# Kernel tuning notes

Measured on AMD Instinct MI355X. Metric: run time of the kernel, lower is better.

The kernel has to match this reference:

```python
import jax, jax.numpy as jnp
import numpy as np

N_NODES = 50000
N_EDGES = 800000
IN_DIM = 128
HID = 128
OUT_DIM = 64
NUM_GRAPHS = 512
GM_P = 2.0
EPS = 1e-6


def setup_inputs() -> dict:
    key = jax.random.key(0)
    ks = jax.random.split(key, 12)
    x = jax.random.normal(ks[0], (N_NODES, IN_DIM), dtype=jnp.float32)
    edge_index = jax.random.randint(ks[1], (2, N_EDGES), 0, N_NODES, dtype=jnp.int64)
    batch = jnp.sort(jax.random.randint(ks[2], (N_NODES,), 0, NUM_GRAPHS, dtype=jnp.int64))
    def lin(k, fan_in, fan_out):
        w = jax.random.normal(k, (fan_in, fan_out), dtype=jnp.float32) / np.sqrt(fan_in)
        return w
    return {
        "x": x,
        "edge_index": edge_index,
        "batch": batch,
        # 3 GCN conv layers (weight + bias each)
        "W0": lin(ks[3], IN_DIM, HID), "b0": jnp.zeros((HID,), jnp.float32),
        "W1": lin(ks[4], HID, HID),    "b1": jnp.zeros((HID,), jnp.float32),
        "W2": lin(ks[5], HID, HID),    "b2": jnp.zeros((HID,), jnp.float32),
        # 2 FF layers: [HID->HID], [HID->OUT_DIM]
        "Wf0": lin(ks[6], HID, HID),   "bf0": jnp.zeros((HID,), jnp.float32),
        "Wf1": lin(ks[7], HID, OUT_DIM), "bf1": jnp.zeros((OUT_DIM,), jnp.float32),
    }


def _gcn_layer(h, src, dst, deg_inv_sqrt, W, b):
    # PyG GCNConv: h' = D^-1/2 (A + I) D^-1/2 (h W) + b, deg includes self-loop
    h = h @ W                                           # [N, F]
    norm = deg_inv_sqrt[src] * deg_inv_sqrt[dst]        # [E]
    msg = h[src] * norm[:, None]                        # gather + scale, [E, F]
    agg = jax.ops.segment_sum(msg, dst, num_segments=N_NODES)
    agg = agg + h * (deg_inv_sqrt * deg_inv_sqrt)[:, None]   # self-loop term (norm = 1/deg)
    return agg + b


def _gm_pool(x, batch, p):
    # sign-preserving generalized mean pool via scatter_mean
    xt = jnp.sign(x) * (jnp.abs(x) + EPS) ** p
    sums = jax.ops.segment_sum(xt, batch, num_segments=NUM_GRAPHS)
    cnt = jax.ops.segment_sum(jnp.ones((x.shape[0],), x.dtype), batch, num_segments=NUM_GRAPHS)
    pooled = sums / jnp.maximum(cnt, 1.0)[:, None]
    return jnp.sign(pooled) * (jnp.abs(pooled) + EPS) ** (1.0 / p)


def reference(x, edge_index, batch, W0, b0, W1, b1, W2, b2, Wf0, bf0, Wf1, bf1):
    src, dst = edge_index[0], edge_index[1]
    # degree of aggregation targets, with +1 for self-loops (computed once; graph is static)
    deg = jax.ops.segment_sum(jnp.ones((N_EDGES,), x.dtype), dst, num_segments=N_NODES) + 1.0
    deg_inv_sqrt = jax.lax.rsqrt(deg)

    h = _gcn_layer(x, src, dst, deg_inv_sqrt, W0, b0)
    h = jax.nn.relu(h)
    h = _gcn_layer(h, src, dst, deg_inv_sqrt, W1, b1)
    h = jax.nn.relu(h)
    h = _gcn_layer(h, src, dst, deg_inv_sqrt, W2, b2)  # no relu after last conv

    graph_repr = _gm_pool(h, batch, GM_P)              # [G, HID]
    graph_repr = jax.nn.relu(graph_repr)

    z = jax.nn.relu(graph_repr @ Wf0 + bf0)
    logits = z @ Wf1 + bf1                             # [G, OUT_DIM]
    return logits
```

## Files before the change

### kernel.cpp

```cpp
#include <hip/hip_runtime.h>

#define N_NODES   50000
#define M_PAD     50048
#define N_TILES   1564
#define GEMM_GRID 391
#define N_EDGES   800000
#define HID       128
#define OUT_DIM   64
#define NUM_GRAPHS 512
#define EPS       1e-6f
#define NBUCK     196
#define BUCKCAP   6144
#define ABLOCKS   98

typedef __attribute__((ext_vector_type(8))) short short8;
typedef __attribute__((ext_vector_type(4))) float f32x4;
typedef __attribute__((ext_vector_type(16))) float f32x16;

static __device__ __forceinline__ unsigned short f2bf(float f) {
    unsigned u = __builtin_bit_cast(unsigned, f);
    u += 0x7FFFu + ((u >> 16) & 1u);
    return (unsigned short)(u >> 16);
}
static __device__ __forceinline__ float bf2f(unsigned short h) {
    unsigned u = ((unsigned)h) << 16;
    return __builtin_bit_cast(float, u);
}

static __device__ __forceinline__ float signpow(float x, bool sqrt_mode) {
    if (x == 0.0f) return 0.0f;
    float a = fabsf(x) + EPS;
    float v = sqrt_mode ? sqrtf(a) : a * a;
    return x > 0.0f ? v : -v;
}

__global__ __launch_bounds__(256) void k_bucketize(const int* __restrict__ ei,
                                                   int* __restrict__ gcnt,
                                                   unsigned* __restrict__ ebuf) {
    __shared__ int lcnt[NBUCK];
    __shared__ int lbase[NBUCK];
    int tid = threadIdx.x;
    for (int i = tid; i < NBUCK; i += 256) lcnt[i] = 0;
    __syncthreads();

    const uint4* src4 = (const uint4*)ei;
    const uint4* dst4 = (const uint4*)(ei + N_EDGES);
    int base4 = blockIdx.x * 2048;

    #pragma unroll 1
    for (int it = 0; it < 8; it++) {
        int i4 = base4 + it * 256 + tid;
        if (i4 < N_EDGES / 4) {
            uint4 d = dst4[i4];
            atomicAdd(&lcnt[d.x >> 8], 1);
            atomicAdd(&lcnt[d.y >> 8], 1);
            atomicAdd(&lcnt[d.z >> 8], 1);
            atomicAdd(&lcnt[d.w >> 8], 1);
        }
    }
    __syncthreads();
    for (int i = tid; i < NBUCK; i += 256) {
        lbase[i] = atomicAdd(&gcnt[i], lcnt[i]);
        lcnt[i] = 0;
    }
    __syncthreads();

    #pragma unroll 1
    for (int it = 0; it < 8; it++) {
        int i4 = base4 + it * 256 + tid;
        if (i4 < N_EDGES / 4) {
            uint4 d = dst4[i4];
            uint4 s = src4[i4];
            unsigned dd[4] = {d.x, d.y, d.z, d.w};
            unsigned ss[4] = {s.x, s.y, s.z, s.w};
            #pragma unroll
            for (int k = 0; k < 4; k++) {
                int b = dd[k] >> 8;
                int p = atomicAdd(&lcnt[b], 1);
                ebuf[(size_t)b * BUCKCAP + lbase[b] + p] = ss[k] | (dd[k] << 16);
            }
        }
    }
}

__global__ __launch_bounds__(256) void k_bscan(const int* __restrict__ gcnt,
                                               int* __restrict__ bbase,
                                               int* __restrict__ offs) {
    __shared__ int sm[256];
    int t = threadIdx.x;
    int v = (t < NBUCK) ? gcnt[t] : 0;
    sm[t] = v;
    __syncthreads();
    for (int off = 1; off < 256; off <<= 1) {
        int u = (t >= off) ? sm[t - off] : 0;
        __syncthreads();
        sm[t] += u;
        __syncthreads();
    }
    if (t < NBUCK) bbase[t] = sm[t] - v;
    if (t == 0) { bbase[NBUCK] = N_EDGES; offs[N_NODES] = N_EDGES; }
}

__global__ __launch_bounds__(256) void k_csr(const unsigned* __restrict__ ebuf,
                                             const int* __restrict__ gcnt,
                                             const int* __restrict__ bbase,
                                             int* __restrict__ offs,
                                             float* __restrict__ dis,
                                             int* __restrict__ csr) {
    __shared__ int cntA[256];
    __shared__ int scanA[256];
    int b = blockIdx.x;
    int t = threadIdx.x;
    int n0 = b * 256;
    int count = gcnt[b];
    int base  = bbase[b];
    const unsigned* eb = ebuf + (size_t)b * BUCKCAP;

    cntA[t] = 0;
    __syncthreads();
    for (int i = t; i < count; i += 256)
        atomicAdd(&cntA[eb[i] >> 16 & 0xFF], 1);
    __syncthreads();
    int c = cntA[t];
    scanA[t] = c;
    __syncthreads();
    for (int off = 1; off < 256; off <<= 1) {
        int u = (t >= off) ? scanA[t - off] : 0;
        __syncthreads();
        scanA[t] += u;
        __syncthreads();
    }
    int excl = scanA[t] - c;
    int n = n0 + t;
    if (n < N_NODES) {
        offs[n] = base + excl;
        dis[n]  = rsqrtf((float)c + 1.0f);
    }
    scanA[t] = excl;
    cntA[t] = 0;
    __syncthreads();
    for (int i = t; i < count; i += 256) {
        unsigned v = eb[i];
        int ln = (v >> 16) & 0xFF;
        int p = atomicAdd(&cntA[ln], 1);
        csr[base + scanA[ln] + p] = (int)(v & 0xFFFFu);
    }
}

__global__ void k_split(const float* __restrict__ in, short* __restrict__ hi,
                        short* __restrict__ lo, int n4) {
    int i = blockIdx.x * blockDim.x + threadIdx.x;
    if (i >= n4) return;
    float4 v = ((const float4*)in)[i];
    unsigned short h0 = f2bf(v.x), h1 = f2bf(v.y), h2 = f2bf(v.z), h3 = f2bf(v.w);
    unsigned short l0 = f2bf(v.x - bf2f(h0)), l1 = f2bf(v.y - bf2f(h1));
    unsigned short l2 = f2bf(v.z - bf2f(h2)), l3 = f2bf(v.w - bf2f(h3));
    ushort4 vh; vh.x = h0; vh.y = h1; vh.z = h2; vh.w = h3;
    ushort4 vl; vl.x = l0; vl.y = l1; vl.z = l2; vl.w = l3;
    ((ushort4*)hi)[i] = vh;
    ((ushort4*)lo)[i] = vl;
}

__global__ void k_wsplit3(const float* __restrict__ W0, const float* __restrict__ W1,
                          const float* __restrict__ W2, short* __restrict__ Wth,
                          short* __restrict__ Wtl) {
    int which = blockIdx.y;
    const float* W = which == 0 ? W0 : (which == 1 ? W1 : W2);
    int tid = blockIdx.x * blockDim.x + threadIdx.x;
    int k = tid & 127, n = tid >> 7;
    float w = W[k * HID + n];
    unsigned short h = f2bf(w);
    Wth[which * HID * HID + n * HID + k] = (short)h;
    Wtl[which * HID * HID + n * HID + k] = (short)f2bf(w - bf2f(h));
}

__global__ __launch_bounds__(256) void k_gemm_mfma(const short* __restrict__ Ah,
                                                   const short* __restrict__ Al,
                                                   const short* __restrict__ Wh,
                                                   const short* __restrict__ Wl,
                                                   unsigned short* __restrict__ th,
                                                   unsigned short* __restrict__ tl,
                                                   const float* __restrict__ scale) {
    __shared__ short As_h[32 * 128];
    __shared__ short As_l[32 * 128];
    int tid  = threadIdx.x;
    int lane = tid & 63;
    int col  = (tid >> 6) * 32 + (lane & 31);
    int kh   = lane >> 5;
    int r    = lane & 31;

    short8 bh[8], bl[8];
    #pragma unroll
    for (int ks = 0; ks < 8; ks++) {
        bh[ks] = *(const short8*)(Wh + (size_t)col * HID + ks * 16 + kh * 8);
        bl[ks] = *(const short8*)(Wl + (size_t)col * HID + ks * 16 + kh * 8);
    }

    int su0 = tid, su1 = tid + 256;
    int sr0 = su0 >> 4, sc0 = su0 & 15;
    int sr1 = su1 >> 4, sc1 = su1 & 15;
    int sw0 = sr0 * 128 + ((sc0 ^ (sr0 & 7)) * 8);
    int sw1 = sr1 * 128 + ((sc1 ^ (sr1 & 7)) * 8);

    for (int tile = blockIdx.x; tile < N_TILES; tile += GEMM_GRID) {
        int row0 = tile * 32;
        __syncthreads();
        {
            const short* gh = Ah + (size_t)row0 * HID;
            const short* gl = Al + (size_t)row0 * HID;
            *(short8*)&As_h[sw0] = *(const short8*)(gh + sr0 * HID + sc0 * 8);
            *(short8*)&As_h[sw1] = *(const short8*)(gh + sr1 * HID + sc1 * 8);
            *(short8*)&As_l[sw0] = *(const short8*)(gl + sr0 * HID + sc0 * 8);
            *(short8*)&As_l[sw1] = *(const short8*)(gl + sr1 * HID + sc1 * 8);
        }
        __syncthreads();

        short8 ah[8], al[8];
        #pragma unroll
        for (int ks = 0; ks < 8; ks++) {
            int cg = ks * 2 + kh;
            int off = r * 128 + ((cg ^ (r & 7)) * 8);
            ah[ks] = *(const short8*)&As_h[off];
            al[ks] = *(const short8*)&As_l[off];
        }

        f32x16 acc = {0.f};
        #pragma unroll
        for (int ks = 0; ks < 8; ks++) {
            acc = __builtin_amdgcn_mfma_f32_32x32x16_bf16(ah[ks], bh[ks], acc, 0, 0, 0);
            acc = __builtin_amdgcn_mfma_f32_32x32x16_bf16(al[ks], bh[ks], acc, 0, 0, 0);
            acc = __builtin_amdgcn_mfma_f32_32x32x16_bf16(ah[ks], bl[ks], acc, 0, 0, 0);
        }

        #pragma unroll
        for (int reg = 0; reg < 16; reg++) {
            int row = row0 + (reg & 3) + 8 * (reg >> 2) + 4 * kh;
            float v = acc[reg] * scale[row];
            unsigned short hi = f2bf(v);
            th[(size_t)row * HID + col] = hi;
            tl[(size_t)row * HID + col] = f2bf(v - bf2f(hi));
        }
    }
}

__global__ __launch_bounds__(256) void k_agg(const unsigned short* __restrict__ th,
                                             const unsigned short* __restrict__ tl,
                                             const int* __restrict__ offs,
                                             const int* __restrict__ csr_src,
                                             const float* __restrict__ dis,
                                             const float* __restrict__ bias,
                                             float* __restrict__ hout,
                                             short* __restrict__ hh,
                                             short* __restrict__ hl,
                                             int mode) {
    int node = blockIdx.x * 4 + (threadIdx.x >> 6);
    if (node >= N_NODES) return;
    int lane = threadIdx.x & 63;
    int c  = lane & 31;
    int e  = lane >> 5;
    int beg = offs[node], end = offs[node + 1];
    float dn = dis[node];

    float ax[4] = {}, ay[4] = {}, az[4] = {}, aw[4] = {};
    for (int j = beg; j < end; j += 8) {
        #pragma unroll
        for (int k = 0; k < 4; k++) {
            int jj = j + k * 2 + e;
            int jc = jj < end ? jj : end - 1;
            int s = csr_src[jc];
            float m = (jj < end) ? 1.0f : 0.0f;
            uint2 v = *(const uint2*)&th[(size_t)s * HID + c * 4];
            float v0 = __builtin_bit_cast(float, v.x << 16);
            float v1 = __builtin_bit_cast(float, v.x & 0xFFFF0000u);
            float v2 = __builtin_bit_cast(float, v.y << 16);
            float v3 = __builtin_bit_cast(float, v.y & 0xFFFF0000u);
            ax[k] = fmaf(v0, m, ax[k]);
            ay[k] = fmaf(v1, m, ay[k]);
            az[k] = fmaf(v2, m, az[k]);
            aw[k] = fmaf(v3, m, aw[k]);
        }
    }
    float tx = (ax[0] + ax[1]) + (ax[2] + ax[3]);
    float ty = (ay[0] + ay[1]) + (ay[2] + ay[3]);
    float tz = (az[0] + az[1]) + (az[2] + az[3]);
    float tw = (aw[0] + aw[1]) + (aw[2] + aw[3]);
    tx += __shfl_xor(tx, 32);
    ty += __shfl_xor(ty, 32);
    tz += __shfl_xor(tz, 32);
    tw += __shfl_xor(tw, 32);

    if (e == 0) {
        ushort4 sh = *(const ushort4*)&th[(size_t)node * HID + c * 4];
        ushort4 sl = *(const ushort4*)&tl[(size_t)node * HID + c * 4];
        float4 b4  = *(const float4*)&bias[c * 4];
        float ox = (tx + bf2f(sh.x) + bf2f(sl.x)) * dn + b4.x;
        float oy = (ty + bf2f(sh.y) + bf2f(sl.y)) * dn + b4.y;
        float oz = (tz + bf2f(sh.z) + bf2f(sl.z)) * dn + b4.z;
        float ow = (tw + bf2f(sh.w) + bf2f(sl.w)) * dn + b4.w;
        if (mode == 1) {
            ox = fmaxf(ox, 0.f); oy = fmaxf(oy, 0.f);
            oz = fmaxf(oz, 0.f); ow = fmaxf(ow, 0.f);
            unsigned short hx = f2bf(ox), hy = f2bf(oy), hz = f2bf(oz), hw = f2bf(ow);
            ushort4 vh; vh.x = hx; vh.y = hy; vh.z = hz; vh.w = hw;
            ushort4 vl;
            vl.x = f2bf(ox - bf2f(hx)); vl.y = f2bf(oy - bf2f(hy));
            vl.z = f2bf(oz - bf2f(hz)); vl.w = f2bf(ow - bf2f(hw));
            *(ushort4*)&hh[(size_t)node * HID + c * 4] = vh;
            *(ushort4*)&hl[(size_t)node * HID + c * 4] = vl;
        } else {
            float4 o = make_float4(ox, oy, oz, ow);
            *(float4*)&hout[(size_t)node * HID + c * 4] = o;
        }
    }
}

__global__ void k_bounds(const int* __restrict__ batch, int* __restrict__ gstart) {
    int n = blockIdx.x * blockDim.x + threadIdx.x;
    if (n >= N_NODES) return;
    int b  = batch[n];
    int bp = (n == 0) ? -1 : batch[n - 1];
    for (int g = bp + 1; g <= b; g++) gstart[g] = n;
    if (n == N_NODES - 1)
        for (int g = b + 1; g <= NUM_GRAPHS; g++) gstart[g] = N_NODES;
}

__global__ __launch_bounds__(256) void k_pool(const float* __restrict__ h,
                                              const int* __restrict__ gstart,
                                              float* __restrict__ pooled) {
    __shared__ float smx[4][64], smy[4][64];
    int g = blockIdx.x;
    int t = threadIdx.x;
    int c = t & 63;
    int slot = t >> 6;
    int beg = gstart[g], end = gstart[g + 1];

    float sx = 0.f, sy = 0.f;
    for (int n = beg + slot; n < end; n += 4) {
        float2 v = *(const float2*)&h[(size_t)n * HID + c * 2];
        sx += signpow(v.x, false);
        sy += signpow(v.y, false);
    }
    smx[slot][c] = sx; smy[slot][c] = sy;
    __syncthreads();
    if (slot == 0) {
        sx = (smx[0][c] + smx[1][c]) + (smx[2][c] + smx[3][c]);
        sy = (smy[0][c] + smy[1][c]) + (smy[2][c] + smy[3][c]);
        float cnt = fmaxf((float)(end - beg), 1.0f);
        float px = sx / cnt, py = sy / cnt;
        pooled[g * HID + c * 2]     = fmaxf(signpow(px, true), 0.f);
        pooled[g * HID + c * 2 + 1] = fmaxf(signpow(py, true), 0.f);
    }
}

__global__ __launch_bounds__(128) void k_ff(const float* __restrict__ pooled,
                                            const float* __restrict__ Wf0,
                                            const float* __restrict__ bf0,
                                            const float* __restrict__ Wf1,
                                            const float* __restrict__ bf1,
                                            float* __restrict__ out) {
    __shared__ float row[128];
    __shared__ float zrow[128];
    int g = blockIdx.x, t = threadIdx.x;
    row[t] = pooled[g * HID + t];
    __syncthreads();
    float acc = bf0[t];
    #pragma unroll 8
    for (int k = 0; k < 128; k++) acc = fmaf(row[k], Wf0[k * 128 + t], acc);
    zrow[t] = fmaxf(acc, 0.f);
    __syncthreads();
    if (t < OUT_DIM) {
        float a2 = bf1[t];
        #pragma unroll 8
        for (int k = 0; k < 128; k++) a2 = fmaf(zrow[k], Wf1[k * OUT_DIM + t], a2);
        out[g * OUT_DIM + t] = a2;
    }
}

static inline size_t align256(size_t x) { return (x + 255) & ~(size_t)255; }

extern "C" void kernel_launch(void* const* d_in, const int* in_sizes, int n_in,
                              void* d_out, int out_size, void* d_ws, size_t ws_size,
                              hipStream_t stream) {
    const float* x     = (const float*)d_in[0];
    const int*   ei    = (const int*)d_in[1];
    const int*   batch = (const int*)d_in[2];
    const float* W0  = (const float*)d_in[3];  const float* b0  = (const float*)d_in[4];
    const float* W1  = (const float*)d_in[5];  const float* b1  = (const float*)d_in[6];
    const float* W2  = (const float*)d_in[7];  const float* b2  = (const float*)d_in[8];
    const float* Wf0 = (const float*)d_in[9];  const float* bf0 = (const float*)d_in[10];
    const float* Wf1 = (const float*)d_in[11]; const float* bf1 = (const float*)d_in[12];
    float* out = (float*)d_out;

    char* p = (char*)d_ws;
    unsigned short* th = (unsigned short*)p; p += align256((size_t)M_PAD * HID * 2);
    unsigned short* tl = (unsigned short*)p; p += align256((size_t)M_PAD * HID * 2);
    short* bufAh = (short*)p; p += align256((size_t)M_PAD * HID * 2);
    short* bufAl = (short*)p; p += align256((size_t)M_PAD * HID * 2);
    short* bufBh = (short*)p; p += align256((size_t)M_PAD * HID * 2);
    short* bufBl = (short*)p; p += align256((size_t)M_PAD * HID * 2);
    float* h     = (float*)bufBh;
    unsigned* ebuf = (unsigned*)p; p += align256((size_t)NBUCK * BUCKCAP * 4);
    int*   gcnt    = (int*)p;   p += align256((size_t)NBUCK * 4);
    int*   bbase   = (int*)p;   p += align256((size_t)(NBUCK + 1) * 4);
    int*   offs    = (int*)p;   p += align256((size_t)(N_NODES + 1) * 4);
    int*   csr     = (int*)p;   p += align256((size_t)N_EDGES * 4);
    float* dis     = (float*)p; p += align256((size_t)N_NODES * 4);
    int*   gstart  = (int*)p;   p += align256((size_t)(NUM_GRAPHS + 1) * 4);
    float* pooled  = (float*)p; p += align256((size_t)NUM_GRAPHS * HID * 4);
    short* Wth     = (short*)p; p += align256((size_t)3 * HID * HID * 2);
    short* Wtl     = (short*)p; p += align256((size_t)3 * HID * HID * 2);

    hipMemsetAsync(gcnt, 0, (size_t)NBUCK * 4, stream);

    const int TB = 256;
    k_bucketize<<<ABLOCKS, 256, 0, stream>>>(ei, gcnt, ebuf);
    k_bscan    <<<1, 256, 0, stream>>>(gcnt, bbase, offs);
    k_csr      <<<NBUCK, 256, 0, stream>>>(ebuf, gcnt, bbase, offs, dis, csr);

    int n4 = N_NODES * HID / 4;
    k_split<<<(n4 + TB - 1) / TB, TB, 0, stream>>>(x, bufAh, bufAl, n4);
    dim3 wg(64, 3);
    k_wsplit3<<<wg, 256, 0, stream>>>(W0, W1, W2, Wth, Wtl);

    int agg_blocks = (N_NODES + 3) / 4;

    k_gemm_mfma<<<GEMM_GRID, 256, 0, stream>>>(bufAh, bufAl, Wth, Wtl, th, tl, dis);
    k_agg<<<agg_blocks, 256, 0, stream>>>(th, tl, offs, csr, dis, b0,
                                          nullptr, bufBh, bufBl, 1);
    k_gemm_mfma<<<GEMM_GRID, 256, 0, stream>>>(bufBh, bufBl, Wth + HID * HID, Wtl + HID * HID,
                                               th, tl, dis);
    k_agg<<<agg_blocks, 256, 0, stream>>>(th, tl, offs, csr, dis, b1,
                                          nullptr, bufAh, bufAl, 1);
    k_gemm_mfma<<<GEMM_GRID, 256, 0, stream>>>(bufAh, bufAl, Wth + 2 * HID * HID, Wtl + 2 * HID * HID,
                                               th, tl, dis);
    k_agg<<<agg_blocks, 256, 0, stream>>>(th, tl, offs, csr, dis, b2,
                                          h, nullptr, nullptr, 0);

    k_bounds<<<(N_NODES + TB - 1) / TB, TB, 0, stream>>>(batch, gstart);
    k_pool<<<NUM_GRAPHS, 256, 0, stream>>>(h, gstart, pooled);
    k_ff<<<NUM_GRAPHS, 128, 0, stream>>>(pooled, Wf0, bf0, Wf1, bf1, out);
}
```

Baseline: 227.6 us.

## Fuse preprocessing kernels, drop low-bf16 GEMM output, fuse pool and FF

```diff
diff --git a/kernel.cpp b/kernel.cpp
--- a/kernel.cpp
+++ b/kernel.cpp
@@ -3,7 +3,7 @@
 #define N_NODES   50000
 #define M_PAD     50048
 #define N_TILES   1564
-#define GEMM_GRID 391
+#define GEMM_GRID 782
 #define N_EDGES   800000
 #define HID       128
 #define OUT_DIM   64
@@ -14,7 +14,6 @@
 #define ABLOCKS   98
 
 typedef __attribute__((ext_vector_type(8))) short short8;
-typedef __attribute__((ext_vector_type(4))) float f32x4;
 typedef __attribute__((ext_vector_type(16))) float f32x16;
 
 static __device__ __forceinline__ unsigned short f2bf(float f) {
@@ -83,37 +82,31 @@
     }
 }
 
-__global__ __launch_bounds__(256) void k_bscan(const int* __restrict__ gcnt,
-                                               int* __restrict__ bbase,
-                                               int* __restrict__ offs) {
-    __shared__ int sm[256];
-    int t = threadIdx.x;
-    int v = (t < NBUCK) ? gcnt[t] : 0;
-    sm[t] = v;
-    __syncthreads();
-    for (int off = 1; off < 256; off <<= 1) {
-        int u = (t >= off) ? sm[t - off] : 0;
-        __syncthreads();
-        sm[t] += u;
-        __syncthreads();
-    }
-    if (t < NBUCK) bbase[t] = sm[t] - v;
-    if (t == 0) { bbase[NBUCK] = N_EDGES; offs[N_NODES] = N_EDGES; }
-}
-
 __global__ __launch_bounds__(256) void k_csr(const unsigned* __restrict__ ebuf,
                                              const int* __restrict__ gcnt,
-                                             const int* __restrict__ bbase,
                                              int* __restrict__ offs,
                                              float* __restrict__ dis,
                                              int* __restrict__ csr) {
     __shared__ int cntA[256];
     __shared__ int scanA[256];
+    __shared__ int sbase;
     int b = blockIdx.x;
     int t = threadIdx.x;
     int n0 = b * 256;
+
+    int v = (t < NBUCK) ? gcnt[t] : 0;
+    scanA[t] = v;
+    __syncthreads();
+    for (int off = 1; off < 256; off <<= 1) {
+        int u = (t >= off) ? scanA[t - off] : 0;
+        __syncthreads();
+        scanA[t] += u;
+        __syncthreads();
+    }
+    if (t == 0) sbase = (b == 0) ? 0 : scanA[b - 1];
+    __syncthreads();
+    int base  = sbase;
     int count = gcnt[b];
-    int base  = bbase[b];
     const unsigned* eb = ebuf + (size_t)b * BUCKCAP;
 
     cntA[t] = 0;
@@ -136,29 +129,16 @@
         offs[n] = base + excl;
         dis[n]  = rsqrtf((float)c + 1.0f);
     }
+    if (b == 0 && t == 0) offs[N_NODES] = N_EDGES;
     scanA[t] = excl;
     cntA[t] = 0;
     __syncthreads();
     for (int i = t; i < count; i += 256) {
-        unsigned v = eb[i];
-        int ln = (v >> 16) & 0xFF;
+        unsigned vv = eb[i];
+        int ln = (vv >> 16) & 0xFF;
         int p = atomicAdd(&cntA[ln], 1);
-        csr[base + scanA[ln] + p] = (int)(v & 0xFFFFu);
-    }
-}
-
-__global__ void k_split(const float* __restrict__ in, short* __restrict__ hi,
-                        short* __restrict__ lo, int n4) {
-    int i = blockIdx.x * blockDim.x + threadIdx.x;
-    if (i >= n4) return;
-    float4 v = ((const float4*)in)[i];
-    unsigned short h0 = f2bf(v.x), h1 = f2bf(v.y), h2 = f2bf(v.z), h3 = f2bf(v.w);
-    unsigned short l0 = f2bf(v.x - bf2f(h0)), l1 = f2bf(v.y - bf2f(h1));
-    unsigned short l2 = f2bf(v.z - bf2f(h2)), l3 = f2bf(v.w - bf2f(h3));
-    ushort4 vh; vh.x = h0; vh.y = h1; vh.z = h2; vh.w = h3;
-    ushort4 vl; vl.x = l0; vl.y = l1; vl.z = l2; vl.w = l3;
-    ((ushort4*)hi)[i] = vh;
-    ((ushort4*)lo)[i] = vl;
+        csr[base + scanA[ln] + p] = (int)(vv & 0xFFFFu);
+    }
 }
 
 __global__ void k_wsplit3(const float* __restrict__ W0, const float* __restrict__ W1,
@@ -174,12 +154,12 @@
     Wtl[which * HID * HID + n * HID + k] = (short)f2bf(w - bf2f(h));
 }
 
-__global__ __launch_bounds__(256) void k_gemm_mfma(const short* __restrict__ Ah,
-                                                   const short* __restrict__ Al,
+template<int FP32SRC>
+__global__ __launch_bounds__(256) void k_gemm_mfma(const void* __restrict__ Asrc_h,
+                                                   const void* __restrict__ Asrc_l,
                                                    const short* __restrict__ Wh,
                                                    const short* __restrict__ Wl,
                                                    unsigned short* __restrict__ th,
-                                                   unsigned short* __restrict__ tl,
                                                    const float* __restrict__ scale) {
     __shared__ short As_h[32 * 128];
     __shared__ short As_l[32 * 128];
@@ -205,9 +185,29 @@
     for (int tile = blockIdx.x; tile < N_TILES; tile += GEMM_GRID) {
         int row0 = tile * 32;
         __syncthreads();
-        {
-            const short* gh = Ah + (size_t)row0 * HID;
-            const short* gl = Al + (size_t)row0 * HID;
+        if (FP32SRC) {
+            const float* gx = (const float*)Asrc_h;
+            #pragma unroll
+            for (int u = 0; u < 2; u++) {
+                int sr = u ? sr1 : sr0, sc = u ? sc1 : sc0, sw = u ? sw1 : sw0;
+                int gr = row0 + sr; if (gr >= N_NODES) gr = N_NODES - 1;
+                const float* src = gx + (size_t)gr * HID + sc * 8;
+                float4 a = ((const float4*)src)[0];
+                float4 b = ((const float4*)src)[1];
+                float vals[8] = {a.x, a.y, a.z, a.w, b.x, b.y, b.z, b.w};
+                short8 hi, lo;
+                #pragma unroll
+                for (int j = 0; j < 8; j++) {
+                    unsigned short hh = f2bf(vals[j]);
+                    hi[j] = (short)hh;
+                    lo[j] = (short)f2bf(vals[j] - bf2f(hh));
+                }
+                *(short8*)&As_h[sw] = hi;
+                *(short8*)&As_l[sw] = lo;
+            }
+        } else {
+            const short* gh = (const short*)Asrc_h + (size_t)row0 * HID;
+            const short* gl = (const short*)Asrc_l + (size_t)row0 * HID;
             *(short8*)&As_h[sw0] = *(const short8*)(gh + sr0 * HID + sc0 * 8);
             *(short8*)&As_h[sw1] = *(const short8*)(gh + sr1 * HID + sc1 * 8);
             *(short8*)&As_l[sw0] = *(const short8*)(gl + sr0 * HID + sc0 * 8);
@@ -236,15 +236,12 @@
         for (int reg = 0; reg < 16; reg++) {
             int row = row0 + (reg & 3) + 8 * (reg >> 2) + 4 * kh;
             float v = acc[reg] * scale[row];
-            unsigned short hi = f2bf(v);
-            th[(size_t)row * HID + col] = hi;
-            tl[(size_t)row * HID + col] = f2bf(v - bf2f(hi));
+            th[(size_t)row * HID + col] = f2bf(v);
         }
     }
 }
 
 __global__ __launch_bounds__(256) void k_agg(const unsigned short* __restrict__ th,
-                                             const unsigned short* __restrict__ tl,
                                              const int* __restrict__ offs,
                                              const int* __restrict__ csr_src,
                                              const float* __restrict__ dis,
@@ -291,12 +288,11 @@
 
     if (e == 0) {
         ushort4 sh = *(const ushort4*)&th[(size_t)node * HID + c * 4];
-        ushort4 sl = *(const ushort4*)&tl[(size_t)node * HID + c * 4];
         float4 b4  = *(const float4*)&bias[c * 4];
-        float ox = (tx + bf2f(sh.x) + bf2f(sl.x)) * dn + b4.x;
-        float oy = (ty + bf2f(sh.y) + bf2f(sl.y)) * dn + b4.y;
-        float oz = (tz + bf2f(sh.z) + bf2f(sl.z)) * dn + b4.z;
-        float ow = (tw + bf2f(sh.w) + bf2f(sl.w)) * dn + b4.w;
+        float ox = (tx + bf2f(sh.x)) * dn + b4.x;
+        float oy = (ty + bf2f(sh.y)) * dn + b4.y;
+        float oz = (tz + bf2f(sh.z)) * dn + b4.z;
+        float ow = (tw + bf2f(sh.w)) * dn + b4.w;
         if (mode == 1) {
             ox = fmaxf(ox, 0.f); oy = fmaxf(oy, 0.f);
             oz = fmaxf(oz, 0.f); ow = fmaxf(ow, 0.f);
@@ -314,26 +310,31 @@
     }
 }
 
-__global__ void k_bounds(const int* __restrict__ batch, int* __restrict__ gstart) {
-    int n = blockIdx.x * blockDim.x + threadIdx.x;
-    if (n >= N_NODES) return;
-    int b  = batch[n];
-    int bp = (n == 0) ? -1 : batch[n - 1];
-    for (int g = bp + 1; g <= b; g++) gstart[g] = n;
-    if (n == N_NODES - 1)
-        for (int g = b + 1; g <= NUM_GRAPHS; g++) gstart[g] = N_NODES;
-}
-
-__global__ __launch_bounds__(256) void k_pool(const float* __restrict__ h,
-                                              const int* __restrict__ gstart,
-                                              float* __restrict__ pooled) {
+__global__ __launch_bounds__(256) void k_poolff(const float* __restrict__ h,
+                                                const int* __restrict__ batch,
+                                                const float* __restrict__ Wf0,
+                                                const float* __restrict__ bf0,
+                                                const float* __restrict__ Wf1,
+                                                const float* __restrict__ bf1,
+                                                float* __restrict__ out) {
     __shared__ float smx[4][64], smy[4][64];
+    __shared__ float row[128], zrow[128];
+    __shared__ int bnd[2];
     int g = blockIdx.x;
     int t = threadIdx.x;
-    int c = t & 63;
-    int slot = t >> 6;
-    int beg = gstart[g], end = gstart[g + 1];
-
+    if (t < 2) {
+        int target = g + t;
+        int lo = 0, hi = N_NODES;
+        while (lo < hi) {
+            int mid = (lo + hi) >> 1;
+            if (batch[mid] < target) lo = mid + 1; else hi = mid;
+        }
+        bnd[t] = lo;
+    }
+    __syncthreads();
+    int beg = bnd[0], end = bnd[1];
+
+    int c = t & 63, slot = t >> 6;
     float sx = 0.f, sy = 0.f;
     for (int n = beg + slot; n < end; n += 4) {
         float2 v = *(const float2*)&h[(size_t)n * HID + c * 2];
@@ -346,27 +347,16 @@
         sx = (smx[0][c] + smx[1][c]) + (smx[2][c] + smx[3][c]);
         sy = (smy[0][c] + smy[1][c]) + (smy[2][c] + smy[3][c]);
         float cnt = fmaxf((float)(end - beg), 1.0f);
-        float px = sx / cnt, py = sy / cnt;
-        pooled[g * HID + c * 2]     = fmaxf(signpow(px, true), 0.f);
-        pooled[g * HID + c * 2 + 1] = fmaxf(signpow(py, true), 0.f);
-    }
-}
-
-__global__ __launch_bounds__(128) void k_ff(const float* __restrict__ pooled,
-                                            const float* __restrict__ Wf0,
-                                            const float* __restrict__ bf0,
-                                            const float* __restrict__ Wf1,
-                                            const float* __restrict__ bf1,
-                                            float* __restrict__ out) {
-    __shared__ float row[128];
-    __shared__ float zrow[128];
-    int g = blockIdx.x, t = threadIdx.x;
-    row[t] = pooled[g * HID + t];
-    __syncthreads();
-    float acc = bf0[t];
-    #pragma unroll 8
-    for (int k = 0; k < 128; k++) acc = fmaf(row[k], Wf0[k * 128 + t], acc);
-    zrow[t] = fmaxf(acc, 0.f);
+        row[c * 2]     = fmaxf(signpow(sx / cnt, true), 0.f);
+        row[c * 2 + 1] = fmaxf(signpow(sy / cnt, true), 0.f);
+    }
+    __syncthreads();
+    if (t < 128) {
+        float acc = bf0[t];
+        #pragma unroll 8
+        for (int k = 0; k < 128; k++) acc = fmaf(row[k], Wf0[k * 128 + t], acc);
+        zrow[t] = fmaxf(acc, 0.f);
+    }
     __syncthreads();
     if (t < OUT_DIM) {
         float a2 = bf1[t];
@@ -393,7 +383,6 @@
 
     char* p = (char*)d_ws;
     unsigned short* th = (unsigned short*)p; p += align256((size_t)M_PAD * HID * 2);
-    unsigned short* tl = (unsigned short*)p; p += align256((size_t)M_PAD * HID * 2);
     short* bufAh = (short*)p; p += align256((size_t)M_PAD * HID * 2);
     short* bufAl = (short*)p; p += align256((size_t)M_PAD * HID * 2);
     short* bufBh = (short*)p; p += align256((size_t)M_PAD * HID * 2);
@@ -401,42 +390,33 @@
     float* h     = (float*)bufBh;
     unsigned* ebuf = (unsigned*)p; p += align256((size_t)NBUCK * BUCKCAP * 4);
     int*   gcnt    = (int*)p;   p += align256((size_t)NBUCK * 4);
-    int*   bbase   = (int*)p;   p += align256((size_t)(NBUCK + 1) * 4);
     int*   offs    = (int*)p;   p += align256((size_t)(N_NODES + 1) * 4);
     int*   csr     = (int*)p;   p += align256((size_t)N_EDGES * 4);
     float* dis     = (float*)p; p += align256((size_t)N_NODES * 4);
-    int*   gstart  = (int*)p;   p += align256((size_t)(NUM_GRAPHS + 1) * 4);
-    float* pooled  = (float*)p; p += align256((size_t)NUM_GRAPHS * HID * 4);
     short* Wth     = (short*)p; p += align256((size_t)3 * HID * HID * 2);
     short* Wtl     = (short*)p; p += align256((size_t)3 * HID * HID * 2);
 
     hipMemsetAsync(gcnt, 0, (size_t)NBUCK * 4, stream);
 
-    const int TB = 256;
     k_bucketize<<<ABLOCKS, 256, 0, stream>>>(ei, gcnt, ebuf);
-    k_bscan    <<<1, 256, 0, stream>>>(gcnt, bbase, offs);
-    k_csr      <<<NBUCK, 256, 0, stream>>>(ebuf, gcnt, bbase, offs, dis, csr);
-
-    int n4 = N_NODES * HID / 4;
-    k_split<<<(n4 + TB - 1) / TB, TB, 0, stream>>>(x, bufAh, bufAl, n4);
+    k_csr      <<<NBUCK, 256, 0, stream>>>(ebuf, gcnt, offs, dis, csr);
+
     dim3 wg(64, 3);
     k_wsplit3<<<wg, 256, 0, stream>>>(W0, W1, W2, Wth, Wtl);
 
     int agg_blocks = (N_NODES + 3) / 4;
 
-    k_gemm_mfma<<<GEMM_GRID, 256, 0, stream>>>(bufAh, bufAl, Wth, Wtl, th, tl, dis);
-    k_agg<<<agg_blocks, 256, 0, stream>>>(th, tl, offs, csr, dis, b0,
+    k_gemm_mfma<1><<<GEMM_GRID, 256, 0, stream>>>(x, nullptr, Wth, Wtl, th, dis);
+    k_agg<<<agg_blocks, 256, 0, stream>>>(th, offs, csr, dis, b0,
                                           nullptr, bufBh, bufBl, 1);
-    k_gemm_mfma<<<GEMM_GRID, 256, 0, stream>>>(bufBh, bufBl, Wth + HID * HID, Wtl + HID * HID,
-                                               th, tl, dis);
-    k_agg<<<agg_blocks, 256, 0, stream>>>(th, tl, offs, csr, dis, b1,
+    k_gemm_mfma<0><<<GEMM_GRID, 256, 0, stream>>>(bufBh, bufBl,
+                                                  Wth + HID * HID, Wtl + HID * HID, th, dis);
+    k_agg<<<agg_blocks, 256, 0, stream>>>(th, offs, csr, dis, b1,
                                           nullptr, bufAh, bufAl, 1);
-    k_gemm_mfma<<<GEMM_GRID, 256, 0, stream>>>(bufAh, bufAl, Wth + 2 * HID * HID, Wtl + 2 * HID * HID,
-                                               th, tl, dis);
-    k_agg<<<agg_blocks, 256, 0, stream>>>(th, tl, offs, csr, dis, b2,
+    k_gemm_mfma<0><<<GEMM_GRID, 256, 0, stream>>>(bufAh, bufAl,
+                                                  Wth + 2 * HID * HID, Wtl + 2 * HID * HID, th, dis);
+    k_agg<<<agg_blocks, 256, 0, stream>>>(th, offs, csr, dis, b2,
                                           h, nullptr, nullptr, 0);
 
-    k_bounds<<<(N_NODES + TB - 1) / TB, TB, 0, stream>>>(batch, gstart);
-    k_pool<<<NUM_GRAPHS, 256, 0, stream>>>(h, gstart, pooled);
-    k_ff<<<NUM_GRAPHS, 128, 0, stream>>>(pooled, Wf0, bf0, Wf1, bf1, out);
-}
+    k_poolff<<<NUM_GRAPHS, 256, 0, stream>>>(h, batch, Wf0, bf0, Wf1, bf1, out);
+}
```

Result: faster. 206.3 us (-9.3%).
